# Kernel optimization log

Measured on AMD Instinct MI355X. Metric: run time of the kernel, lower is better.

The kernel has to match this reference:

```python
import jax, jax.numpy as jnp
import numpy as np

HIDDEN = 1024
HEADS = 16
HEAD_DIM = HIDDEN // HEADS  # 64
ROPE_DIM = 64
ROPE_BASE = 10000.0
B, T = 2, 2048


def setup_inputs() -> dict:
    key = jax.random.key(0)
    k1, k2, k3, k4, k5, k6 = jax.random.split(key, 6)
    x = jax.random.normal(k1, (B, T, HIDDEN), dtype=jnp.float32)
    input_ids = jax.random.randint(k2, (B, T), 0, 32000)
    # torch Linear weights: [out_features, in_features]
    qkv_w = jax.random.normal(k3, (3 * HIDDEN, HIDDEN), dtype=jnp.float32) * (1.0 / np.sqrt(HIDDEN))
    qkv_b = jnp.zeros((3 * HIDDEN,), dtype=jnp.float32)
    out_w = jax.random.normal(k4, (HIDDEN, HIDDEN), dtype=jnp.float32) * (1.0 / np.sqrt(HIDDEN))
    out_b = jnp.zeros((HIDDEN,), dtype=jnp.float32)
    global_idx = jnp.array([0, 1, 2], dtype=jnp.int64)  # special_tokens values
    return {"x": x, "input_ids": input_ids, "qkv_w": qkv_w, "qkv_b": qkv_b,
            "out_w": out_w, "out_b": out_b, "global_idx": global_idx}


def _rope_cos_sin(t, offset=0):
    inv_freq = 1.0 / (ROPE_BASE ** (jnp.arange(0, ROPE_DIM, 2, dtype=jnp.float32) / ROPE_DIM))  # [ROPE_DIM/2]
    pos = jnp.arange(offset, offset + t, dtype=jnp.float32)
    freqs = pos[:, None] * inv_freq[None, :]  # [T, ROPE_DIM/2]
    return jnp.cos(freqs)[None, None], jnp.sin(freqs)[None, None]  # [1,1,T,ROPE_DIM/2]


def _apply_rotary(x, cos, sin):
    x_rot, x_pass = x[..., :ROPE_DIM], x[..., ROPE_DIM:]
    half = ROPE_DIM // 2
    x1, x2 = x_rot[..., :half], x_rot[..., half:]
    return jnp.concatenate([x1 * cos - x2 * sin, x1 * sin + x2 * cos, x_pass], axis=-1)


def reference(x, input_ids, qkv_w, qkv_b, out_w, out_b, global_idx):
    b, t, _ = x.shape
    qkv = x @ qkv_w.T + qkv_b  # [B,T,3*HIDDEN]
    q, k, v = jnp.split(qkv, 3, axis=-1)
    # -> [B, H, T, Dh]
    reshape = lambda z: z.reshape(b, t, HEADS, HEAD_DIM).transpose(0, 2, 1, 3)
    q, k, v = reshape(q), reshape(k), reshape(v)
    cos, sin = _rope_cos_sin(t)
    q = _apply_rotary(q, cos, sin)
    k = _apply_rotary(k, cos, sin)
    # causal + global-query mask
    causal = jnp.tril(jnp.ones((t, t), dtype=bool))[None, None]  # [1,1,T,T]
    global_mask = jnp.isin(input_ids, global_idx)  # [B,T]
    allow = causal | global_mask[:, None, :, None]  # [B,1,T,T]
    scale = jnp.sqrt(jnp.float32(HEAD_DIM))
    logits = jnp.einsum('bhqd,bhkd->bhqk', q, k) / scale
    neg = -jnp.finfo(logits.dtype).max
    logits = jnp.where(allow, logits, neg)
    attn = jax.nn.softmax(logits, axis=-1)
    out = jnp.einsum('bhqk,bhkd->bhqd', attn, v)  # [B,H,T,Dh]
    out = out.transpose(0, 2, 1, 3).reshape(b, t, HEADS * HEAD_DIM)
    return out @ out_w.T + out_b
```

## Files before the change

### kernel.cpp

```cpp
#include <hip/hip_runtime.h>
#include <hip/hip_bf16.h>
#include <math.h>

typedef __bf16 bf16;
typedef __bf16 bf16x4 __attribute__((ext_vector_type(4)));
typedef __bf16 bf16x8 __attribute__((ext_vector_type(8)));
typedef float floatx4 __attribute__((ext_vector_type(4)));

#define HIDDEN 1024
#define NHEADS 16
#define HDIM 64
#define TSEQ 2048
#define NBATCH 2
#define MTOT (NBATCH * TSEQ)

__device__ inline void glds16(bf16* lds, const bf16* g)
{
  __builtin_amdgcn_global_load_lds(
      (const __attribute__((address_space(1))) unsigned int*)g,
      (__attribute__((address_space(3))) unsigned int*)lds, 16, 0, 0);
}

__global__ __launch_bounds__(256) void prep_kernel(
    const float* __restrict__ x, bf16* __restrict__ xb,
    const float* __restrict__ qkv_w, bf16* __restrict__ qkv_wb,
    float2* __restrict__ rope)
{
  const int bid = blockIdx.x;
  if (bid >= 3584) {
    const int e0 = ((bid - 3584) * 256 + threadIdx.x) * 4;
    const int t = e0 >> 5;
    const int d2 = e0 & 31;
#pragma unroll
    for (int j = 0; j < 4; j++) {
      const float inv = exp2f((float)(d2 + j) * -0.41524100f);
      float s, c;
      sincosf((float)t * inv, &s, &c);
      rope[e0 + j] = make_float2(c, s);
    }
    return;
  }
  const float* src = (bid < 2048) ? x : qkv_w;
  bf16* dst = (bid < 2048) ? xb : qkv_wb;
  const int i = (((bid < 2048) ? bid : bid - 2048) * 256 + threadIdx.x) * 8;
  const floatx4 u = *(const floatx4*)(src + i);
  const floatx4 v = *(const floatx4*)(src + i + 4);
  bf16x8 r;
#pragma unroll
  for (int j = 0; j < 4; j++) { r[j] = (bf16)u[j]; r[4 + j] = (bf16)v[j]; }
  *(bf16x8*)(dst + i) = r;
}

__global__ __launch_bounds__(256) void cvt_f32_bf16(
    const float* __restrict__ src, bf16* __restrict__ dst, int n)
{
  const int i = (blockIdx.x * 256 + threadIdx.x) * 8;
  if (i >= n) return;
  const floatx4 u = *(const floatx4*)(src + i);
  const floatx4 v = *(const floatx4*)(src + i + 4);
  bf16x8 r;
#pragma unroll
  for (int j = 0; j < 4; j++) { r[j] = (bf16)u[j]; r[4 + j] = (bf16)v[j]; }
  *(bf16x8*)(dst + i) = r;
}

__global__ __launch_bounds__(512, 2) void gemm_qkv(
    const bf16* __restrict__ A, const bf16* __restrict__ W,
    const float* __restrict__ bias, const float2* __restrict__ rope,
    bf16* __restrict__ Qb, bf16* __restrict__ Kb, bf16* __restrict__ Vt,
    int M, int N, int K)
{
  __shared__ bf16 As[2][2][256 * 32];
  __shared__ bf16 Bs[2][2][256 * 32];

  const int tid  = threadIdx.x;
  const int lane = tid & 63;
  const int wv   = tid >> 6;
  const int quad = lane >> 4;
  const int l16  = lane & 15;
  const int wm   = (wv >> 2) * 128;
  const int wn   = (wv & 3) * 64;

  const int f   = blockIdx.x;
  const int xcd = f & 7;
  const int rr  = f >> 3;
  const int bx  = (xcd & 1) * 6 + rr % 6;
  const int by  = (xcd >> 1) * 4 + rr / 6;
  const int m0 = by * 256;
  const int n0 = bx * 256;

  const int srow = lane >> 2;
  const int scol = ((lane & 3) ^ ((lane >> 3) & 3)) * 8;
  const int qsw  = (quad ^ ((l16 >> 1) & 3)) * 8;

  const bf16* gaBase = A + (size_t)(m0 + wv * 16 + srow) * K + scol;
  const bf16* gbBase = W + (size_t)(n0 + wv * 16 + srow) * K + scol;
  const int ldst = wv * 512 + lane * 8;

#define STG_A(d, kh, kcol)                                                   \
  glds16(&As[d][kh][ldst],        gaBase + (kcol));                          \
  glds16(&As[d][kh][ldst + 4096], gaBase + (size_t)128 * K + (kcol));
#define STG_B(d, kh, kcol)                                                   \
  glds16(&Bs[d][kh][ldst],        gbBase + (kcol));                          \
  glds16(&Bs[d][kh][ldst + 4096], gbBase + (size_t)128 * K + (kcol));

#define RD_PH(d, kh, mh)                                                     \
  _Pragma("unroll") for (int i = 0; i < 4; i++)                              \
    af[i] = *(const bf16x8*)(&As[d][kh][(wm + (mh) * 64 + i * 16 + l16) * 32 + qsw]); \
  _Pragma("unroll") for (int j = 0; j < 4; j++)                              \
    bfr[j] = *(const bf16x8*)(&Bs[d][kh][(wn + j * 16 + l16) * 32 + qsw]);

#define MM_PH(mh)                                                            \
  _Pragma("unroll") for (int i = 0; i < 4; i++)                              \
    _Pragma("unroll") for (int j = 0; j < 4; j++)                            \
      acc[(mh) * 4 + i][j] = __builtin_amdgcn_mfma_f32_16x16x32_bf16(        \
          af[i], bfr[j], acc[(mh) * 4 + i][j], 0, 0, 0);

  floatx4 acc[8][4];
#pragma unroll
  for (int i = 0; i < 8; i++)
#pragma unroll
    for (int j = 0; j < 4; j++) acc[i][j] = (floatx4){0.f, 0.f, 0.f, 0.f};

  STG_A(0, 0, 0); STG_B(0, 0, 0);
  STG_A(0, 1, 32); STG_B(0, 1, 32);
  asm volatile("s_waitcnt vmcnt(4)" ::: "memory");
  __builtin_amdgcn_s_barrier();

  const int nt = K >> 6;
#pragma unroll 1
  for (int t = 0; t < nt; t++) {
    const int c = t & 1;
    const int kn = (t + 1) * 64;
    const bool more = (t + 1 < nt);
    bf16x8 af[4], bfr[4];

    RD_PH(c, 0, 0);
    if (more) { STG_A(c ^ 1, 0, kn); }
    __builtin_amdgcn_s_barrier();
    __builtin_amdgcn_s_setprio(1); MM_PH(0); __builtin_amdgcn_s_setprio(0);

    RD_PH(c, 0, 1);
    if (more) {
      STG_B(c ^ 1, 0, kn);
      asm volatile("s_waitcnt vmcnt(4)" ::: "memory");
    } else {
      asm volatile("s_waitcnt vmcnt(0)" ::: "memory");
    }
    __builtin_amdgcn_s_barrier();
    __builtin_amdgcn_s_setprio(1); MM_PH(1); __builtin_amdgcn_s_setprio(0);

    RD_PH(c, 1, 0);
    if (more) { STG_A(c ^ 1, 1, kn + 32); }
    __builtin_amdgcn_s_barrier();
    __builtin_amdgcn_s_setprio(1); MM_PH(0); __builtin_amdgcn_s_setprio(0);

    RD_PH(c, 1, 1);
    if (more) {
      STG_B(c ^ 1, 1, kn + 32);
      asm volatile("s_waitcnt vmcnt(4)" ::: "memory");
    }
    __builtin_amdgcn_s_barrier();
    __builtin_amdgcn_s_setprio(1); MM_PH(1); __builtin_amdgcn_s_setprio(0);
  }

  const int sect = n0 >> 10;
  const int hw   = ((n0 & 1023) + wn) >> 6;

  float bs[4];
#pragma unroll
  for (int j = 0; j < 4; j++) bs[j] = bias[n0 + wn + j * 16 + l16];

  if (sect < 2) {
    bf16* dst = sect ? Kb : Qb;
#pragma unroll
    for (int i = 0; i < 8; i++) {
      const int gmBase = m0 + wm + i * 16 + quad * 4;
#pragma unroll
      for (int r = 0; r < 4; r++) {
        const int gm = gmBase + r;
        const int b_ = gm >> 11, t = gm & 2047;
        const size_t rowbase = ((size_t)(b_ * NHEADS + hw) * TSEQ + t) * HDIM;
        const float2 cs0 = rope[t * 32 + l16];
        const float2 cs1 = rope[t * 32 + 16 + l16];
        const float x1a = acc[i][0][r] + bs[0];
        const float x2a = acc[i][2][r] + bs[2];
        const float x1b = acc[i][1][r] + bs[1];
        const float x2b = acc[i][3][r] + bs[3];
        dst[rowbase + l16]      = (bf16)(x1a * cs0.x - x2a * cs0.y);
        dst[rowbase + 32 + l16] = (bf16)(x1a * cs0.y + x2a * cs0.x);
        dst[rowbase + 16 + l16] = (bf16)(x1b * cs1.x - x2b * cs1.y);
        dst[rowbase + 48 + l16] = (bf16)(x1b * cs1.y + x2b * cs1.x);
      }
    }
  } else {
#pragma unroll
    for (int j = 0; j < 4; j++) {
      const int d = j * 16 + l16;
#pragma unroll
      for (int i = 0; i < 8; i++) {
        const int gmBase = m0 + wm + i * 16 + quad * 4;
        const int b_ = gmBase >> 11, t0 = gmBase & 2047;
        bf16x4 vv;
#pragma unroll
        for (int r = 0; r < 4; r++) vv[r] = (bf16)(acc[i][j][r] + bs[j]);
        *(bf16x4*)(Vt + ((size_t)((b_ * NHEADS + hw) * HDIM + d)) * TSEQ + t0) = vv;
      }
    }
  }
}

__global__ __launch_bounds__(256) void gemm_out(
    const bf16* __restrict__ A, const bf16* __restrict__ W,
    const float* __restrict__ bias, float* __restrict__ C,
    int M, int N, int K)
{
  __shared__ bf16 As2[3][128 * 32];
  __shared__ bf16 Bs2[3][64 * 32];

  const int tid  = threadIdx.x;
  const int lane = tid & 63;
  const int wv   = tid >> 6;
  const int quad = lane >> 4;
  const int l16  = lane & 15;

  const int f   = blockIdx.x;
  const int xcd = f & 7;
  const int rr  = f >> 3;
  const int bx  = (xcd & 1) * 8 + (rr & 7);
  const int by  = (xcd >> 1) * 8 + (rr >> 3);
  const int m0 = by * 128;
  const int n0 = bx * 64;
  const int wm = wv * 32;

  const int srow = lane >> 2;
  const int scol = ((lane & 3) ^ ((lane >> 3) & 3)) * 8;
  const int qsw  = (quad ^ ((l16 >> 1) & 3)) * 8;

  const bf16* ga0 = A + (size_t)(m0 + wv * 32 + srow) * K + scol;
  const bf16* gb0 = W + (size_t)(n0 + wv * 16 + srow) * K + scol;

  floatx4 acc[2][4];
#pragma unroll
  for (int i = 0; i < 2; i++)
#pragma unroll
    for (int j = 0; j < 4; j++) acc[i][j] = (floatx4){0.f, 0.f, 0.f, 0.f};

#define STAGE_O(buf, kk)                                                    \
  glds16(&As2[buf][(wv * 32) * 32], ga0 + (kk));                            \
  glds16(&As2[buf][(wv * 32 + 16) * 32], ga0 + (size_t)16 * K + (kk));      \
  glds16(&Bs2[buf][(wv * 16) * 32], gb0 + (kk));

#define COMPUTE_O(buf)                                                      \
  {                                                                         \
    bf16x8 af[2], bfr[4];                                                   \
    _Pragma("unroll") for (int i = 0; i < 2; i++)                           \
        af[i] = *(const bf16x8*)(&As2[buf][(wm + i * 16 + l16) * 32 + qsw]);\
    _Pragma("unroll") for (int j = 0; j < 4; j++)                           \
        bfr[j] = *(const bf16x8*)(&Bs2[buf][(j * 16 + l16) * 32 + qsw]);    \
    _Pragma("unroll") for (int i = 0; i < 2; i++)                           \
        _Pragma("unroll") for (int j = 0; j < 4; j++)                       \
            acc[i][j] = __builtin_amdgcn_mfma_f32_16x16x32_bf16(            \
                af[i], bfr[j], acc[i][j], 0, 0, 0);                         \
  }

  STAGE_O(0, 0);
  STAGE_O(1, 32);
  int cur = 0;
  const int nsteps = K / 32;
#pragma unroll 1
  for (int t = 0; t < nsteps - 1; t++) {
    asm volatile("s_waitcnt vmcnt(3)" ::: "memory");
    __builtin_amdgcn_s_barrier();
    if (t + 2 < nsteps) {
      const int nb = (cur >= 1) ? cur - 1 : cur + 2;
      STAGE_O(nb, (t + 2) * 32);
    }
    COMPUTE_O(cur);
    cur = (cur == 2) ? 0 : cur + 1;
  }
  asm volatile("s_waitcnt vmcnt(0)" ::: "memory");
  __builtin_amdgcn_s_barrier();
  COMPUTE_O(cur);

#pragma unroll
  for (int i = 0; i < 2; i++) {
    const int gmBase = m0 + wm + i * 16 + quad * 4;
#pragma unroll
    for (int j = 0; j < 4; j++) {
      const int gn = n0 + j * 16 + l16;
      const float bsv = bias[gn];
#pragma unroll
      for (int r = 0; r < 4; r++)
        C[(size_t)(gmBase + r) * N + gn] = acc[i][j][r] + bsv;
    }
  }
}

__device__ inline int swz(int g) { return (g & ~7) | ((g ^ (g >> 3) ^ (g >> 6)) & 7); }

__global__ __launch_bounds__(256) void attn_kernel(
    const bf16* __restrict__ Q, const bf16* __restrict__ K,
    const bf16* __restrict__ Vt, bf16* __restrict__ O,
    const int* __restrict__ ids, const int* __restrict__ gidx)
{
  __shared__ bf16 Ks[4096];
  __shared__ bf16 Vs[4096];
  __shared__ int flags[4];

  const int tid  = threadIdx.x;
  const int lane = tid & 63;
  const int wv   = tid >> 6;
  const int quad = lane >> 4;
  const int l16  = lane & 15;

  const int xcd = blockIdx.x & 7;
  const int j   = blockIdx.x >> 3;
  const int bh  = xcd * 4 + (j >> 4);
  const int p   = j & 15;
  const int b  = bh >> 4;
  const int h  = bh & 15;

  const bf16* Qp = Q + (size_t)bh * TSEQ * HDIM;
  const bf16* Kp = K + (size_t)bh * TSEQ * HDIM;
  const bf16* Vp = Vt + (size_t)bh * HDIM * TSEQ;

  const int rK  = tid >> 3;
  const int dcK = tid & 7;
  const int gk = ((rK >> 2) & 1) * 128 + (dcK >> 2) * 64 +
                 ((dcK & 3) * 16 + (((rK >> 3) << 2) | (rK & 3)));
  const int kd0 = swz(gk) * 8, kd1 = swz(gk + 256) * 8;
  const int dV = tid >> 3;
  const int uV = tid & 7;
  const int gv = (uV >> 2) * 256 + (dV >> 4) * 64 + ((uV & 3) * 16 + (dV & 15));
  const int vd0 = swz(gv) * 8, vd1 = swz(gv + 128) * 8;

  const int g0v = gidx[0], g1v = gidx[1], g2v = gidx[2];

#pragma unroll
  for (int ph = 0; ph < 2; ph++) {
    const int qt = ph ? p : (31 - p);
    const int q0 = qt * 64 + wv * 16;

    const bf16x8 qf0 = *(const bf16x8*)(Qp + (size_t)(q0 + l16) * HDIM + quad * 8);
    const bf16x8 qf1 = *(const bf16x8*)(Qp + (size_t)(q0 + l16) * HDIM + 32 + quad * 8);

    const int myq = q0 + l16;
    const int myid = ids[b * TSEQ + myq];
    const int gl = (myid == g0v) | (myid == g1v) | (myid == g2v);
    flags[wv] = __any(gl);
    __syncthreads();
    const int anyg = flags[0] | flags[1] | flags[2] | flags[3];
    const int kmax = anyg ? TSEQ : (qt * 64 + 64);

    float lsum = 0.f;
    floatx4 o[4];
#pragma unroll
    for (int nt = 0; nt < 4; nt++) o[nt] = (floatx4){0.f, 0.f, 0.f, 0.f};

    bf16x8 kA = *(const bf16x8*)(Kp + tid * 8);
    bf16x8 kB = *(const bf16x8*)(Kp + 2048 + tid * 8);
    bf16x8 vA = *(const bf16x8*)(Vp + (size_t)dV * TSEQ + uV * 8);
    bf16x8 vB = *(const bf16x8*)(Vp + (size_t)(dV + 32) * TSEQ + uV * 8);

    for (int k0 = 0; k0 < kmax; k0 += 64) {
      __syncthreads();
      *(bf16x8*)(Ks + kd0) = kA;
      *(bf16x8*)(Ks + kd1) = kB;
      *(bf16x8*)(Vs + vd0) = vA;
      *(bf16x8*)(Vs + vd1) = vB;
      __syncthreads();

      if (k0 + 64 < kmax) {
        const bf16* kc = Kp + (size_t)(k0 + 64) * HDIM;
        kA = *(const bf16x8*)(kc + tid * 8);
        kB = *(const bf16x8*)(kc + 2048 + tid * 8);
        vA = *(const bf16x8*)(Vp + (size_t)dV * TSEQ + k0 + 64 + uV * 8);
        vB = *(const bf16x8*)(Vp + (size_t)(dV + 32) * TSEQ + k0 + 64 + uV * 8);
      }

#pragma unroll
      for (int g = 0; g < 2; g++) {
        const int kb = k0 + g * 32;
        const int rb = g * 256 + lane;
        const bf16x8 a00 = *(const bf16x8*)(Ks + swz(rb) * 8);
        const bf16x8 a01 = *(const bf16x8*)(Ks + swz(rb + 64) * 8);
        const bf16x8 a10 = *(const bf16x8*)(Ks + swz(rb + 128) * 8);
        const bf16x8 a11 = *(const bf16x8*)(Ks + swz(rb + 192) * 8);
        floatx4 s0 = (floatx4){0.f, 0.f, 0.f, 0.f};
        floatx4 s1 = (floatx4){0.f, 0.f, 0.f, 0.f};
        s0 = __builtin_amdgcn_mfma_f32_16x16x32_bf16(a00, qf0, s0, 0, 0, 0);
        s0 = __builtin_amdgcn_mfma_f32_16x16x32_bf16(a01, qf1, s0, 0, 0, 0);
        s1 = __builtin_amdgcn_mfma_f32_16x16x32_bf16(a10, qf0, s1, 0, 0, 0);
        s1 = __builtin_amdgcn_mfma_f32_16x16x32_bf16(a11, qf1, s1, 0, 0, 0);

        bf16x8 pf;
#pragma unroll
        for (int r = 0; r < 4; r++) {
          const int key0 = kb + quad * 8 + r;
          const int key1 = key0 + 4;
          const float p0 = (gl || key0 <= myq) ? __expf(s0[r] * 0.125f) : 0.f;
          const float p1 = (gl || key1 <= myq) ? __expf(s1[r] * 0.125f) : 0.f;
          lsum += p0 + p1;
          pf[r]     = (bf16)p0;
          pf[4 + r] = (bf16)p1;
        }

#pragma unroll
        for (int nt = 0; nt < 4; nt++) {
          const bf16x8 vf = *(const bf16x8*)(Vs + swz(g * 256 + nt * 64 + lane) * 8);
          o[nt] = __builtin_amdgcn_mfma_f32_16x16x32_bf16(pf, vf, o[nt], 0, 0, 0);
        }
      }
    }

    lsum += __shfl_xor(lsum, 16);
    lsum += __shfl_xor(lsum, 32);

#pragma unroll
    for (int r = 0; r < 4; r++) {
      const float inv = 1.0f / __shfl(lsum, quad * 4 + r);
      const int q = q0 + quad * 4 + r;
      const size_t rowoff = ((size_t)b * TSEQ + q) * HIDDEN + h * HDIM;
#pragma unroll
      for (int nt = 0; nt < 4; nt++)
        O[rowoff + nt * 16 + l16] = (bf16)(o[nt][r] * inv);
    }
  }
}

extern "C" void kernel_launch(void* const* d_in, const int* in_sizes, int n_in,
                              void* d_out, int out_size, void* d_ws, size_t ws_size,
                              hipStream_t stream)
{
  const float* x     = (const float*)d_in[0];
  const int*   ids   = (const int*)d_in[1];
  const float* qkv_w = (const float*)d_in[2];
  const float* qkv_b = (const float*)d_in[3];
  const float* out_w = (const float*)d_in[4];
  const float* out_b = (const float*)d_in[5];
  const int*   gidx  = (const int*)d_in[6];
  float* out = (float*)d_out;

  char* ws = (char*)d_ws;
  bf16* Q      = (bf16*)(ws);
  bf16* Kb     = (bf16*)(ws + (size_t)(8u << 20));
  bf16* Vt     = (bf16*)(ws + (size_t)(16u << 20));
  bf16* slot24 = (bf16*)(ws + (size_t)(24u << 20));
  bf16* xb     = slot24;
  bf16* O      = slot24;
  bf16* out_wb = (bf16*)(ws + (size_t)(16u << 20));
  bf16* qkv_wb = (bf16*)d_out;
  float2* rope = (float2*)((char*)d_out + (size_t)(6u << 20));

  prep_kernel<<<3648, 256, 0, stream>>>(x, xb, qkv_w, qkv_wb, rope);
  gemm_qkv<<<192, 512, 0, stream>>>(
      xb, qkv_wb, qkv_b, rope, Q, Kb, Vt, MTOT, 3 * HIDDEN, HIDDEN);
  attn_kernel<<<512, 256, 0, stream>>>(Q, Kb, Vt, O, ids, gidx);
  cvt_f32_bf16<<<512, 256, 0, stream>>>(out_w, out_wb, HIDDEN * HIDDEN);
  gemm_out<<<512, 256, 0, stream>>>(
      O, out_wb, out_b, out, MTOT, HIDDEN, HIDDEN);
}
```

Before: 189.4 us.

## Split attention key tiles across two wave groups with double-buffered LDS

Attention blocks grow from 4 to 8 waves. Each group of 4 waves processes one 32-key half of every 64-key tile, and the two partial outputs and row sums are merged through LDS at the end. K/V tiles are double-buffered so each iteration needs one barrier instead of two, and each thread loads half as much. This doubles wave-level parallelism per query tile, at the cost of a cross-group reduction, extra barriers and more LDS per block.

```diff
diff --git a/kernel.cpp b/kernel.cpp
--- a/kernel.cpp
+++ b/kernel.cpp
@@ -299,18 +299,20 @@
 
 __device__ inline int swz(int g) { return (g & ~7) | ((g ^ (g >> 3) ^ (g >> 6)) & 7); }
 
-__global__ __launch_bounds__(256) void attn_kernel(
+__global__ __launch_bounds__(512) void attn_kernel(
     const bf16* __restrict__ Q, const bf16* __restrict__ K,
     const bf16* __restrict__ Vt, bf16* __restrict__ O,
     const int* __restrict__ ids, const int* __restrict__ gidx)
 {
-  __shared__ bf16 Ks[4096];
-  __shared__ bf16 Vs[4096];
-  __shared__ int flags[4];
+  __shared__ bf16 Ks[2][4096];
+  __shared__ bf16 Vs[2][4096];
+  __shared__ int flags[8];
 
   const int tid  = threadIdx.x;
   const int lane = tid & 63;
   const int wv   = tid >> 6;
+  const int gg   = wv >> 2;
+  const int w4   = wv & 3;
   const int quad = lane >> 4;
   const int l16  = lane & 15;
 
@@ -325,22 +327,21 @@
   const bf16* Kp = K + (size_t)bh * TSEQ * HDIM;
   const bf16* Vp = Vt + (size_t)bh * HDIM * TSEQ;
 
-  const int rK  = tid >> 3;
-  const int dcK = tid & 7;
-  const int gk = ((rK >> 2) & 1) * 128 + (dcK >> 2) * 64 +
-                 ((dcK & 3) * 16 + (((rK >> 3) << 2) | (rK & 3)));
-  const int kd0 = swz(gk) * 8, kd1 = swz(gk + 256) * 8;
-  const int dV = tid >> 3;
-  const int uV = tid & 7;
+  const int rK2 = tid >> 3, dcK = tid & 7;
+  const int rKl = rK2 & 31, khi = rK2 >> 5;
+  const int gk = ((rKl >> 2) & 1) * 128 + (dcK >> 2) * 64 +
+                 ((dcK & 3) * 16 + (((rKl >> 3) << 2) | (rKl & 3)));
+  const int kd = swz(gk + khi * 256) * 8;
+  const int dV = tid >> 3, uV = tid & 7;
   const int gv = (uV >> 2) * 256 + (dV >> 4) * 64 + ((uV & 3) * 16 + (dV & 15));
-  const int vd0 = swz(gv) * 8, vd1 = swz(gv + 128) * 8;
+  const int vd = swz(gv) * 8;
 
   const int g0v = gidx[0], g1v = gidx[1], g2v = gidx[2];
 
 #pragma unroll
   for (int ph = 0; ph < 2; ph++) {
     const int qt = ph ? p : (31 - p);
-    const int q0 = qt * 64 + wv * 16;
+    const int q0 = qt * 64 + w4 * 16;
 
     const bf16x8 qf0 = *(const bf16x8*)(Qp + (size_t)(q0 + l16) * HDIM + quad * 8);
     const bf16x8 qf1 = *(const bf16x8*)(Qp + (size_t)(q0 + l16) * HDIM + 32 + quad * 8);
@@ -350,7 +351,9 @@
     const int gl = (myid == g0v) | (myid == g1v) | (myid == g2v);
     flags[wv] = __any(gl);
     __syncthreads();
-    const int anyg = flags[0] | flags[1] | flags[2] | flags[3];
+    int anyg = 0;
+#pragma unroll
+    for (int i2 = 0; i2 < 8; i2++) anyg |= flags[i2];
     const int kmax = anyg ? TSEQ : (qt * 64 + 64);
 
     float lsum = 0.f;
@@ -359,73 +362,83 @@
     for (int nt = 0; nt < 4; nt++) o[nt] = (floatx4){0.f, 0.f, 0.f, 0.f};
 
     bf16x8 kA = *(const bf16x8*)(Kp + tid * 8);
-    bf16x8 kB = *(const bf16x8*)(Kp + 2048 + tid * 8);
     bf16x8 vA = *(const bf16x8*)(Vp + (size_t)dV * TSEQ + uV * 8);
-    bf16x8 vB = *(const bf16x8*)(Vp + (size_t)(dV + 32) * TSEQ + uV * 8);
 
     for (int k0 = 0; k0 < kmax; k0 += 64) {
+      bf16* KsB = Ks[(k0 >> 6) & 1];
+      bf16* VsB = Vs[(k0 >> 6) & 1];
+      *(bf16x8*)(KsB + kd) = kA;
+      *(bf16x8*)(VsB + vd) = vA;
       __syncthreads();
-      *(bf16x8*)(Ks + kd0) = kA;
-      *(bf16x8*)(Ks + kd1) = kB;
-      *(bf16x8*)(Vs + vd0) = vA;
-      *(bf16x8*)(Vs + vd1) = vB;
-      __syncthreads();
 
       if (k0 + 64 < kmax) {
-        const bf16* kc = Kp + (size_t)(k0 + 64) * HDIM;
-        kA = *(const bf16x8*)(kc + tid * 8);
-        kB = *(const bf16x8*)(kc + 2048 + tid * 8);
+        kA = *(const bf16x8*)(Kp + (size_t)(k0 + 64) * HDIM + tid * 8);
         vA = *(const bf16x8*)(Vp + (size_t)dV * TSEQ + k0 + 64 + uV * 8);
-        vB = *(const bf16x8*)(Vp + (size_t)(dV + 32) * TSEQ + k0 + 64 + uV * 8);
-      }
-
-#pragma unroll
-      for (int g = 0; g < 2; g++) {
-        const int kb = k0 + g * 32;
-        const int rb = g * 256 + lane;
-        const bf16x8 a00 = *(const bf16x8*)(Ks + swz(rb) * 8);
-        const bf16x8 a01 = *(const bf16x8*)(Ks + swz(rb + 64) * 8);
-        const bf16x8 a10 = *(const bf16x8*)(Ks + swz(rb + 128) * 8);
-        const bf16x8 a11 = *(const bf16x8*)(Ks + swz(rb + 192) * 8);
-        floatx4 s0 = (floatx4){0.f, 0.f, 0.f, 0.f};
-        floatx4 s1 = (floatx4){0.f, 0.f, 0.f, 0.f};
-        s0 = __builtin_amdgcn_mfma_f32_16x16x32_bf16(a00, qf0, s0, 0, 0, 0);
-        s0 = __builtin_amdgcn_mfma_f32_16x16x32_bf16(a01, qf1, s0, 0, 0, 0);
-        s1 = __builtin_amdgcn_mfma_f32_16x16x32_bf16(a10, qf0, s1, 0, 0, 0);
-        s1 = __builtin_amdgcn_mfma_f32_16x16x32_bf16(a11, qf1, s1, 0, 0, 0);
-
-        bf16x8 pf;
-#pragma unroll
-        for (int r = 0; r < 4; r++) {
-          const int key0 = kb + quad * 8 + r;
-          const int key1 = key0 + 4;
-          const float p0 = (gl || key0 <= myq) ? __expf(s0[r] * 0.125f) : 0.f;
-          const float p1 = (gl || key1 <= myq) ? __expf(s1[r] * 0.125f) : 0.f;
-          lsum += p0 + p1;
-          pf[r]     = (bf16)p0;
-          pf[4 + r] = (bf16)p1;
-        }
-
-#pragma unroll
-        for (int nt = 0; nt < 4; nt++) {
-          const bf16x8 vf = *(const bf16x8*)(Vs + swz(g * 256 + nt * 64 + lane) * 8);
-          o[nt] = __builtin_amdgcn_mfma_f32_16x16x32_bf16(pf, vf, o[nt], 0, 0, 0);
-        }
+      }
+
+      const int kb = k0 + gg * 32;
+      const int rb = gg * 256 + lane;
+      const bf16x8 a00 = *(const bf16x8*)(KsB + swz(rb) * 8);
+      const bf16x8 a01 = *(const bf16x8*)(KsB + swz(rb + 64) * 8);
+      const bf16x8 a10 = *(const bf16x8*)(KsB + swz(rb + 128) * 8);
+      const bf16x8 a11 = *(const bf16x8*)(KsB + swz(rb + 192) * 8);
+      floatx4 s0 = (floatx4){0.f, 0.f, 0.f, 0.f};
+      floatx4 s1 = (floatx4){0.f, 0.f, 0.f, 0.f};
+      s0 = __builtin_amdgcn_mfma_f32_16x16x32_bf16(a00, qf0, s0, 0, 0, 0);
+      s0 = __builtin_amdgcn_mfma_f32_16x16x32_bf16(a01, qf1, s0, 0, 0, 0);
+      s1 = __builtin_amdgcn_mfma_f32_16x16x32_bf16(a10, qf0, s1, 0, 0, 0);
+      s1 = __builtin_amdgcn_mfma_f32_16x16x32_bf16(a11, qf1, s1, 0, 0, 0);
+
+      bf16x8 pf;
+#pragma unroll
+      for (int r = 0; r < 4; r++) {
+        const int key0 = kb + quad * 8 + r;
+        const int key1 = key0 + 4;
+        const float p0 = (gl || key0 <= myq) ? __expf(s0[r] * 0.125f) : 0.f;
+        const float p1 = (gl || key1 <= myq) ? __expf(s1[r] * 0.125f) : 0.f;
+        lsum += p0 + p1;
+        pf[r]     = (bf16)p0;
+        pf[4 + r] = (bf16)p1;
+      }
+
+#pragma unroll
+      for (int nt = 0; nt < 4; nt++) {
+        const bf16x8 vf = *(const bf16x8*)(VsB + swz(gg * 256 + nt * 64 + lane) * 8);
+        o[nt] = __builtin_amdgcn_mfma_f32_16x16x32_bf16(pf, vf, o[nt], 0, 0, 0);
       }
     }
 
     lsum += __shfl_xor(lsum, 16);
     lsum += __shfl_xor(lsum, 32);
 
-#pragma unroll
-    for (int r = 0; r < 4; r++) {
-      const float inv = 1.0f / __shfl(lsum, quad * 4 + r);
-      const int q = q0 + quad * 4 + r;
-      const size_t rowoff = ((size_t)b * TSEQ + q) * HIDDEN + h * HDIM;
+    __syncthreads();
+    float* osc = (float*)Ks;
+    float* lsc = (float*)Vs;
+    const int rbase = (w4 * 64 + lane) * 16;
+    if (gg == 1) {
 #pragma unroll
       for (int nt = 0; nt < 4; nt++)
-        O[rowoff + nt * 16 + l16] = (bf16)(o[nt][r] * inv);
-    }
+        *(floatx4*)&osc[rbase + ((nt ^ (lane & 3)) * 4)] = o[nt];
+      lsc[w4 * 64 + lane] = lsum;
+    }
+    __syncthreads();
+    if (gg == 0) {
+      lsum += lsc[w4 * 64 + lane];
+#pragma unroll
+      for (int nt = 0; nt < 4; nt++)
+        o[nt] += *(const floatx4*)&osc[rbase + ((nt ^ (lane & 3)) * 4)];
+
+#pragma unroll
+      for (int r = 0; r < 4; r++) {
+        const float inv = 1.0f / __shfl(lsum, quad * 4 + r);
+        const int q = q0 + quad * 4 + r;
+        const size_t rowoff = ((size_t)b * TSEQ + q) * HIDDEN + h * HDIM;
+#pragma unroll
+        for (int nt = 0; nt < 4; nt++)
+          O[rowoff + nt * 16 + l16] = (bf16)(o[nt][r] * inv);
+      }
+    }
+    __syncthreads();
   }
 }
 
@@ -456,7 +469,7 @@
   prep_kernel<<<3648, 256, 0, stream>>>(x, xb, qkv_w, qkv_wb, rope);
   gemm_qkv<<<192, 512, 0, stream>>>(
       xb, qkv_wb, qkv_b, rope, Q, Kb, Vt, MTOT, 3 * HIDDEN, HIDDEN);
-  attn_kernel<<<512, 256, 0, stream>>>(Q, Kb, Vt, O, ids, gidx);
+  attn_kernel<<<512, 512, 0, stream>>>(Q, Kb, Vt, O, ids, gidx);
   cvt_f32_bf16<<<512, 256, 0, stream>>>(out_w, out_wb, HIDDEN * HIDDEN);
   gemm_out<<<512, 256, 0, stream>>>(
       O, out_wb, out_b, out, MTOT, HIDDEN, HIDDEN);
```

Measured after the change: 182.1 us (median of 2 runs). 3.9% less time.
